# Optimization experiments

Measured on AMD Instinct MI355X. Metric: run time of the kernel, lower is better.

Reference implementation:

```python
import jax, jax.numpy as jnp
import numpy as np
from jax import lax

N, CIN, H, W = 32, 128, 64, 64
COUT, KH, KW = 256, 3, 3
STRIDE = (1, 1)
PADDING = ((1, 1), (1, 1))


def setup_inputs() -> dict:
    key = jax.random.key(0)
    k1, k2, k3, k4 = jax.random.split(key, 4)
    # binary input in {0,1}
    x = jax.random.randint(k1, (N, CIN, H, W), 0, 2).astype(jnp.float32)
    # ternary weight in {-1,0,1}
    weight = (jax.random.randint(k2, (COUT, CIN, KH, KW), 0, 3) - 1).astype(jnp.float32)
    # integer bias (folded from BN, floored to int per get_sign_bias_from_bn)
    bias = jax.random.randint(k3, (COUT,), -200, 200).astype(jnp.float32)
    # sign in {-1,+1}, broadcast shape (1, COUT, 1, 1)
    sign = jnp.where(jax.random.bernoulli(k4, 0.5, (1, COUT, 1, 1)), 1.0, -1.0).astype(jnp.float32)
    return {"x": x, "weight": weight, "bias": bias, "sign": sign}


def reference(x, weight, bias, sign):
    # y = conv2d(x, W) + bias  (stride 1, pad 1, NCHW)
    y = lax.conv_general_dilated(
        x, weight,
        window_strides=STRIDE,
        padding=PADDING,
        dimension_numbers=("NCHW", "OIHW", "NCHW"),
    ) + bias[None, :, None, None]
    # rounding=True -> torch.round_(y)
    y = jnp.round(y)
    # output = 1 iff sign * y >= 0, cast back to input dtype
    return jnp.where(y * sign >= 0, jnp.float32(1), jnp.float32(0)).astype(x.dtype)
```

## Files before the change

kernel.cpp:

```cpp
#include <hip/hip_runtime.h>
#include <cstdint>


#define NIMG 32
#define CIN  128
#define HH   64
#define WW   64
#define COUT 256
#define PH   66
#define X4ROW   4224
#define STG_ROW 8704
#define STG_BYTES (4 * STG_ROW)
#define LDS_TOTAL (STG_BYTES + 4 * X4ROW)
#define WQ4_BYTES ((size_t)9 * 8 * 2 * 64 * 16)

typedef int   v4i  __attribute__((ext_vector_type(4)));
typedef int   v8i  __attribute__((ext_vector_type(8)));
typedef float v16f __attribute__((ext_vector_type(16)));
typedef float v4f  __attribute__((ext_vector_type(4)));

__global__ __launch_bounds__(256) void w_prepack(const float* __restrict__ w,
                                                 int8_t* __restrict__ wq4) {
    const int idx = blockIdx.x * 256 + threadIdx.x;
    if (idx >= (int)WQ4_BYTES) return;
    const int b    = idx & 15;
    const int lane = (idx >> 4) & 63;
    const int s    = (idx >> 10) & 1;
    const int co32 = (idx >> 11) & 7;
    const int tap  = idx >> 14;
    const int co   = co32 * 32 + (lane & 31);
    const int ci0  = s * 64 + (lane >> 5) * 32 + b * 2;
    const int i0 = (int)w[(size_t)(co * CIN + ci0) * 9 + tap];
    const int i1 = (int)w[(size_t)(co * CIN + ci0 + 1) * 9 + tap];
    const uint32_t n0 = (i0 == 0) ? 0u : ((i0 > 0) ? 0x2u : 0xAu);
    const uint32_t n1 = (i1 == 0) ? 0u : ((i1 > 0) ? 0x2u : 0xAu);
    wq4[idx] = (int8_t)(n0 | (n1 << 4));
}

__device__ __forceinline__ v8i widen(v4i x) {
    v8i r = {x[0], x[1], x[2], x[3], 0, 0, 0, 0};
    return r;
}

__global__ __launch_bounds__(512) void binconv_fused(
    const float* __restrict__ x, const int8_t* __restrict__ wq4,
    const float* __restrict__ bias, const float* __restrict__ sign,
    float* __restrict__ out) {

    __shared__ __align__(16) int8_t Smem[LDS_TOTAL];
    int8_t* Stg = Smem;
    int8_t* X4  = Smem + STG_BYTES;

    const int t  = threadIdx.x;
    const int bx = blockIdx.x;
    const int n  = bx >> 5;
    const int y0 = (bx & 31) << 1;

    {
        const int sy = t >> 7;
        const int ci = t & 127;
        const int y  = y0 + sy - 1;
        uint32_t* sp = (uint32_t*)(Stg + sy * STG_ROW + ci * 68);
        if (y >= 0 && y < HH) {
            const float4* xr =
                (const float4*)(x + (((size_t)n * CIN + ci) * HH + y) * WW);
#pragma unroll
            for (int q = 0; q < 16; ++q) {
                float4 v = xr[q];
                const uint32_t b0 = (__float_as_uint(v.x) >> 28) & 2u;
                const uint32_t b1 = (__float_as_uint(v.y) >> 28) & 2u;
                const uint32_t b2 = (__float_as_uint(v.z) >> 28) & 2u;
                const uint32_t b3 = (__float_as_uint(v.w) >> 28) & 2u;
                sp[q] = b0 | (b1 << 8) | (b2 << 16) | (b3 << 24);
            }
        } else {
#pragma unroll
            for (int q = 0; q < 16; ++q) sp[q] = 0u;
        }
    }
    __syncthreads();

    if (t < 264) {
        const int sy  = t / 66;
        const int pxp = t - sy * 66;
        int8_t* dst = X4 + sy * X4ROW + pxp * 64;
        if (pxp == 0 || pxp == 65) {
            const int4 z = {0, 0, 0, 0};
#pragma unroll
            for (int c = 0; c < 4; ++c) *(int4*)(dst + c * 16) = z;
        } else {
            const int8_t* src = Stg + sy * STG_ROW + (pxp - 1);
            uint32_t wrd[16];
#pragma unroll
            for (int k = 0; k < 16; ++k) {
                uint32_t a = 0;
#pragma unroll
                for (int b = 0; b < 4; ++b) {
                    const int j = k * 4 + b;
                    const uint32_t lo = (uint8_t)src[(2 * j)     * 68];
                    const uint32_t hi = (uint8_t)src[(2 * j + 1) * 68];
                    a |= (lo | (hi << 4)) << (8 * b);
                }
                wrd[k] = a;
            }
            const int sk = pxp & 3;
#pragma unroll
            for (int c = 0; c < 4; ++c) {
                int4 vv = {(int)wrd[c*4], (int)wrd[c*4+1],
                           (int)wrd[c*4+2], (int)wrd[c*4+3]};
                *(int4*)(dst + ((c ^ sk) << 4)) = vv;
            }
        }
    }
    __syncthreads();

    const int wid  = t >> 6;
    const int lane = t & 63;
    const int m_lo = lane & 31;
    const int hi   = lane >> 5;
    const int co_off = (wid >> 1) * 64;
    const int yw     = wid & 1;
    const int ct0    = co_off >> 5;

    const int8_t* Xw  = X4 + yw * X4ROW;
    const int8_t* wqb = wq4 + lane * 16;

    v16f acc[2][2] = {};

#pragma unroll
    for (int tap = 0; tap < 9; ++tap) {
        const int ky = tap / 3, kx = tap % 3;
        const int8_t* xl = Xw + ky * X4ROW;
        const int px0 = m_lo + kx;
        const int pk  = px0 & 3;

        v4i af[2][2];
#pragma unroll
        for (int c = 0; c < 2; ++c)
#pragma unroll
            for (int s = 0; s < 2; ++s)
                af[c][s] = *(const v4i*)(wqb
                    + ((((tap * 8 + ct0 + c) * 2) + s) << 10));

        v4i bf[2][2];
#pragma unroll
        for (int s = 0; s < 2; ++s) {
            const int sw = (((s << 1) + hi) ^ pk) << 4;
#pragma unroll
            for (int m = 0; m < 2; ++m)
                bf[m][s] = *(const v4i*)(xl + (px0 + m * 32) * 64 + sw);
        }
#pragma unroll
        for (int s = 0; s < 2; ++s)
#pragma unroll
            for (int c = 0; c < 2; ++c)
#pragma unroll
                for (int m = 0; m < 2; ++m)
                    acc[c][m] = __builtin_amdgcn_mfma_scale_f32_32x32x64_f8f6f4(
                        widen(af[c][s]), widen(bf[m][s]), acc[c][m],
                        4, 4,
                        0, 0x7F7F7F7F,
                        0, 0x7F7F7F7F);
    }

    int8_t* Lep = Smem + wid * 4096;

    const float* bco = bias + co_off;
    const float* sco = sign + co_off;
#pragma unroll
    for (int c = 0; c < 2; ++c) {
#pragma unroll
        for (int r = 0; r < 16; ++r) {
            const int co_l = c * 32 + (r & 3) + 8 * (r >> 2) + 4 * hi;
            const float bv = bco[co_l];
            const float sv = sco[co_l];
#pragma unroll
            for (int m = 0; m < 2; ++m) {
                const float yv = acc[c][m][r] + bv;
                const bool on = (sv > 0.0f) ? (yv >= 0.0f) : (yv <= 0.0f);
                Lep[co_l * 64 + m * 32 + m_lo] = (int8_t)on;
            }
        }
    }
    const int r16 = lane & 15, q4 = lane >> 4;
    float* outb = out + ((size_t)n * COUT + co_off) * (HH * WW)
                + (y0 + yw) * WW;
#pragma unroll
    for (int g = 0; g < 16; ++g) {
        const int p = g * 4 + q4;
        const uint32_t u = *(const uint32_t*)&Lep[p * 64 + r16 * 4];
        v4f v;
        v.x = (float)( u        & 0xff);
        v.y = (float)((u >>  8) & 0xff);
        v.z = (float)((u >> 16) & 0xff);
        v.w = (float)((u >> 24) & 0xff);
        __builtin_nontemporal_store(v,
            (v4f*)(outb + (size_t)p * (HH * WW) + r16 * 4));
    }
}

__global__ __launch_bounds__(256) void naive_conv(
    const float* __restrict__ x, const float* __restrict__ w,
    const float* __restrict__ bias, const float* __restrict__ sign,
    float* __restrict__ out) {
    const int idx = blockIdx.x * 256 + threadIdx.x;
    const int xc = idx & 63, y = (idx >> 6) & 63, co = (idx >> 12) & 255,
              n = idx >> 20;
    float s = 0.f;
    for (int ci = 0; ci < CIN; ++ci)
        for (int ky = 0; ky < 3; ++ky) {
            const int iy = y + ky - 1;
            if (iy < 0 || iy >= HH) continue;
            for (int kx = 0; kx < 3; ++kx) {
                const int ix = xc + kx - 1;
                if (ix < 0 || ix >= WW) continue;
                s += x[((size_t)(n * CIN + ci) * HH + iy) * WW + ix] *
                     w[((size_t)(co * CIN + ci) * 3 + ky) * 3 + kx];
            }
        }
    const float yv = s + bias[co];
    out[idx] = ((sign[co] > 0.f) ? (yv >= 0.f) : (yv <= 0.f)) ? 1.0f : 0.0f;
}

extern "C" void kernel_launch(void* const* d_in, const int* in_sizes, int n_in,
                              void* d_out, int out_size, void* d_ws, size_t ws_size,
                              hipStream_t stream) {
    const float* x    = (const float*)d_in[0];
    const float* w    = (const float*)d_in[1];
    const float* bias = (const float*)d_in[2];
    const float* sign = (const float*)d_in[3];
    float* out = (float*)d_out;

    if (ws_size < WQ4_BYTES) {
        naive_conv<<<dim3((NIMG * COUT * HH * WW) / 256), 256, 0, stream>>>(
            x, w, bias, sign, out);
        return;
    }
    int8_t* wq4 = (int8_t*)d_ws;

    w_prepack<<<dim3((int)((WQ4_BYTES + 255) / 256)), 256, 0, stream>>>(w, wq4);
    binconv_fused<<<dim3(NIMG * (HH / 2)), 512, 0, stream>>>(
        x, wq4, bias, sign, out);
}
```

Before: 207.5 us.

## Pack channel pairs in staging and store epilogue directly without LDS transpose

The input staging phase now has 256 threads each read two channels and pack both into nibble-paired bytes, so the staging buffer is half the size and the repack step reads 4 bytes per output word instead of 8. The epilogue drops the LDS round trip and stores each scalar result straight to global memory with nontemporal stores. This is meant to cut LDS traffic and synchronisation. The cost is that output writes become 4-byte scalar stores, 32 lanes contiguous, instead of 16-byte vector stores, and only half the threads now do the global loads.

```diff
diff --git a/kernel.cpp b/kernel.cpp
--- a/kernel.cpp
+++ b/kernel.cpp
@@ -7,17 +7,15 @@
 #define HH   64
 #define WW   64
 #define COUT 256
-#define PH   66
 #define X4ROW   4224
-#define STG_ROW 8704
-#define STG_BYTES (4 * STG_ROW)
+#define STG_SY  4352
+#define STG_BYTES (4 * STG_SY)
 #define LDS_TOTAL (STG_BYTES + 4 * X4ROW)
 #define WQ4_BYTES ((size_t)9 * 8 * 2 * 64 * 16)
 
 typedef int   v4i  __attribute__((ext_vector_type(4)));
 typedef int   v8i  __attribute__((ext_vector_type(8)));
 typedef float v16f __attribute__((ext_vector_type(16)));
-typedef float v4f  __attribute__((ext_vector_type(4)));
 
 __global__ __launch_bounds__(256) void w_prepack(const float* __restrict__ w,
                                                  int8_t* __restrict__ wq4) {
@@ -56,22 +54,24 @@
     const int n  = bx >> 5;
     const int y0 = (bx & 31) << 1;
 
-    {
-        const int sy = t >> 7;
-        const int ci = t & 127;
+    if (t < 256) {
+        const int sy = t >> 6;
+        const int pr = t & 63;
         const int y  = y0 + sy - 1;
-        uint32_t* sp = (uint32_t*)(Stg + sy * STG_ROW + ci * 68);
+        uint32_t* sp = (uint32_t*)(Stg + sy * STG_SY + pr * 68);
         if (y >= 0 && y < HH) {
-            const float4* xr =
-                (const float4*)(x + (((size_t)n * CIN + ci) * HH + y) * WW);
+            const uint4* r0 =
+                (const uint4*)(x + (((size_t)n * CIN + 2 * pr)     * HH + y) * WW);
+            const uint4* r1 =
+                (const uint4*)(x + (((size_t)n * CIN + 2 * pr + 1) * HH + y) * WW);
 #pragma unroll
             for (int q = 0; q < 16; ++q) {
-                float4 v = xr[q];
-                const uint32_t b0 = (__float_as_uint(v.x) >> 28) & 2u;
-                const uint32_t b1 = (__float_as_uint(v.y) >> 28) & 2u;
-                const uint32_t b2 = (__float_as_uint(v.z) >> 28) & 2u;
-                const uint32_t b3 = (__float_as_uint(v.w) >> 28) & 2u;
-                sp[q] = b0 | (b1 << 8) | (b2 << 16) | (b3 << 24);
+                const uint4 a = r0[q], b = r1[q];
+                uint32_t wd = ((a.x >> 28) & 0x2u)        | ((b.x >> 24) & 0x20u)
+                            | ((a.y >> 20) & 0x200u)      | ((b.y >> 16) & 0x2000u)
+                            | ((a.z >> 12) & 0x20000u)    | ((b.z >> 8) & 0x200000u)
+                            | ((a.w >> 4)  & 0x2000000u)  | ( b.w       & 0x20000000u);
+                sp[q] = wd;
             }
         } else {
 #pragma unroll
@@ -89,19 +89,15 @@
 #pragma unroll
             for (int c = 0; c < 4; ++c) *(int4*)(dst + c * 16) = z;
         } else {
-            const int8_t* src = Stg + sy * STG_ROW + (pxp - 1);
+            const int8_t* src = Stg + sy * STG_SY + (pxp - 1);
             uint32_t wrd[16];
 #pragma unroll
             for (int k = 0; k < 16; ++k) {
-                uint32_t a = 0;
-#pragma unroll
-                for (int b = 0; b < 4; ++b) {
-                    const int j = k * 4 + b;
-                    const uint32_t lo = (uint8_t)src[(2 * j)     * 68];
-                    const uint32_t hi = (uint8_t)src[(2 * j + 1) * 68];
-                    a |= (lo | (hi << 4)) << (8 * b);
-                }
-                wrd[k] = a;
+                const uint32_t b0 = (uint8_t)src[(4 * k + 0) * 68];
+                const uint32_t b1 = (uint8_t)src[(4 * k + 1) * 68];
+                const uint32_t b2 = (uint8_t)src[(4 * k + 2) * 68];
+                const uint32_t b3 = (uint8_t)src[(4 * k + 3) * 68];
+                wrd[k] = b0 | (b1 << 8) | (b2 << 16) | (b3 << 24);
             }
             const int sk = pxp & 3;
 #pragma unroll
@@ -163,10 +159,10 @@
                         0, 0x7F7F7F7F);
     }
 
-    int8_t* Lep = Smem + wid * 4096;
-
     const float* bco = bias + co_off;
     const float* sco = sign + co_off;
+    float* outb = out + ((size_t)n * COUT + co_off) * (HH * WW)
+                + (y0 + yw) * WW + m_lo;
 #pragma unroll
     for (int c = 0; c < 2; ++c) {
 #pragma unroll
@@ -174,28 +170,14 @@
             const int co_l = c * 32 + (r & 3) + 8 * (r >> 2) + 4 * hi;
             const float bv = bco[co_l];
             const float sv = sco[co_l];
+            float* orow = outb + (size_t)co_l * (HH * WW);
 #pragma unroll
             for (int m = 0; m < 2; ++m) {
                 const float yv = acc[c][m][r] + bv;
                 const bool on = (sv > 0.0f) ? (yv >= 0.0f) : (yv <= 0.0f);
-                Lep[co_l * 64 + m * 32 + m_lo] = (int8_t)on;
-            }
-        }
-    }
-    const int r16 = lane & 15, q4 = lane >> 4;
-    float* outb = out + ((size_t)n * COUT + co_off) * (HH * WW)
-                + (y0 + yw) * WW;
-#pragma unroll
-    for (int g = 0; g < 16; ++g) {
-        const int p = g * 4 + q4;
-        const uint32_t u = *(const uint32_t*)&Lep[p * 64 + r16 * 4];
-        v4f v;
-        v.x = (float)( u        & 0xff);
-        v.y = (float)((u >>  8) & 0xff);
-        v.z = (float)((u >> 16) & 0xff);
-        v.w = (float)((u >> 24) & 0xff);
-        __builtin_nontemporal_store(v,
-            (v4f*)(outb + (size_t)p * (HH * WW) + r16 * 4));
+                __builtin_nontemporal_store(on ? 1.0f : 0.0f, orow + m * 32);
+            }
+        }
     }
 }
 
```

Measured after the change: 205.7 us (median of 2 runs). About the same (-0.9%).
